# Optimization experiments

Hardware: AMD Instinct MI355X
Metric: run time of the kernel (lower is better)

Reference implementation:

```python
import jax, jax.numpy as jnp
import numpy as np

B, S, D, H, I = 4, 1024, 2048, 16, 8192
HD = D // H
S_IMG = 576
EPS = 1e-5


def _layer_norm(x, w, b):
    mu = jnp.mean(x, axis=-1, keepdims=True)
    var = jnp.var(x, axis=-1, keepdims=True)
    return (x - mu) * jax.lax.rsqrt(var + EPS) * w + b


def setup_inputs() -> dict:
    key = jax.random.key(0)
    ks = jax.random.split(key, 12)
    s = 0.02
    return {
        "image_features": jax.random.normal(ks[0], (B, S_IMG, D), jnp.float32),
        "hidden_states": jax.random.normal(ks[1], (B, S, D), jnp.float32),
        "attention_mask": jnp.ones((B, S), jnp.float32),
        "causal_attention_mask": jnp.zeros((B, 1, S, S), jnp.float32),
        "Wq": jax.random.normal(ks[2], (D, D), jnp.float32) * s,
        "bq": jnp.zeros((D,), jnp.float32),
        "Wk": jax.random.normal(ks[3], (D, D), jnp.float32) * s,
        "bk": jnp.zeros((D,), jnp.float32),
        "Wv": jax.random.normal(ks[4], (D, D), jnp.float32) * s,
        "bv": jnp.zeros((D,), jnp.float32),
        "Wo": jax.random.normal(ks[5], (D, D), jnp.float32) * s,
        "bo": jnp.zeros((D,), jnp.float32),
        "ln1_w": jnp.ones((D,), jnp.float32),
        "ln1_b": jnp.zeros((D,), jnp.float32),
        "ln2_w": jnp.ones((D,), jnp.float32),
        "ln2_b": jnp.zeros((D,), jnp.float32),
        "W1": jax.random.normal(ks[6], (I, D), jnp.float32) * s,
        "b1": jnp.zeros((I,), jnp.float32),
        "W2": jax.random.normal(ks[7], (D, I), jnp.float32) * s,
        "b2": jnp.zeros((D,), jnp.float32),
    }


def reference(image_features, hidden_states, attention_mask, causal_attention_mask,
              Wq, bq, Wk, bk, Wv, bv, Wo, bo,
              ln1_w, ln1_b, ln2_w, ln2_b, W1, b1, W2, b2):
    dtype = hidden_states.dtype
    scale = HD ** (-0.5)
    # expand_mask: [B,S] -> additive mask [B,1,S,S]
    inverted = 1.0 - attention_mask[:, None, None, :].astype(dtype)  # [B,1,1,S]
    add_mask = jnp.where(inverted.astype(bool), jnp.finfo(dtype).min, inverted)
    add_mask = jnp.broadcast_to(add_mask, (B, 1, S, S))

    residual = hidden_states
    x = _layer_norm(hidden_states, ln1_w, ln1_b)

    q = (x @ Wq.T + bq) * scale
    k = x @ Wk.T + bk
    v = x @ Wv.T + bv
    q = q.reshape(B, S, H, HD)
    k = k.reshape(B, S, H, HD)
    v = v.reshape(B, S, H, HD)

    scores = jnp.einsum('bqhd,bkhd->bhqk', q, k) + add_mask  # [B,H,S,S]
    probs = jax.nn.softmax(scores, axis=-1)
    attn = jnp.einsum('bhqk,bkhd->bqhd', probs, v).reshape(B, S, D)
    attn = attn @ Wo.T + bo

    hidden = residual + attn
    residual = hidden
    y = _layer_norm(hidden, ln2_w, ln2_b)
    y = jax.nn.gelu(y @ W1.T + b1, approximate=False)
    y = y @ W2.T + b2
    return residual + y
```

## Files before the change

kernel.cpp:

```cpp
#include <hip/hip_runtime.h>
#include <hip/hip_bf16.h>
#include <math.h>

typedef __hip_bfloat16 bf16;
typedef __attribute__((ext_vector_type(8))) short short8;
typedef __attribute__((ext_vector_type(4))) float floatx4;

constexpr int Bc = 4, Sc = 1024, Dc = 2048, Hc = 16, HDc = 128, Ic = 8192;
constexpr int QKVLD = 3 * Dc;

__device__ __forceinline__ float bf2f(bf16 x){ return __bfloat162float(x); }
__device__ __forceinline__ bf16 f2bf(float x){ return __float2bfloat16(x); }

__device__ __forceinline__ uint4 pack8(float4 a, float4 b){
    union { uint4 u; bf16 h[8]; } r;
    r.h[0]=f2bf(a.x); r.h[1]=f2bf(a.y); r.h[2]=f2bf(a.z); r.h[3]=f2bf(a.w);
    r.h[4]=f2bf(b.x); r.h[5]=f2bf(b.y); r.h[6]=f2bf(b.z); r.h[7]=f2bf(b.w);
    return r.u;
}

__device__ __forceinline__ void glds16(void* lds, const void* g){
    __builtin_amdgcn_global_load_lds(
        (__attribute__((address_space(1))) void*)(size_t)g,
        (__attribute__((address_space(3))) void*)lds,
        16, 0, 0);
}

__global__ __launch_bounds__(256)
void conv_w(const float* __restrict__ src, bf16* __restrict__ dst){
    const size_t i = ((size_t)blockIdx.x * 256 + threadIdx.x) * 8;
    float4 a = *(const float4*)(src + i);
    float4 b = *(const float4*)(src + i + 4);
    *(uint4*)(dst + i) = pack8(a, b);
}

template<int INF32>
__global__ __launch_bounds__(256)
void ln_kernel(const void* __restrict__ x, const float* __restrict__ w,
               const float* __restrict__ b, bf16* __restrict__ y)
{
    const int row = blockIdx.x;
    const int t = threadIdx.x;
    float f[8], s = 0.f, s2 = 0.f;
    if (INF32) {
        const float* xr = (const float*)x + (size_t)row * Dc + t * 8;
        float4 a = *(const float4*)xr, c = *(const float4*)(xr + 4);
        f[0]=a.x; f[1]=a.y; f[2]=a.z; f[3]=a.w; f[4]=c.x; f[5]=c.y; f[6]=c.z; f[7]=c.w;
    } else {
        union { uint4 u; bf16 h[8]; } ld;
        ld.u = *(const uint4*)((const bf16*)x + (size_t)row * Dc + t * 8);
#pragma unroll
        for (int j = 0; j < 8; ++j) f[j] = bf2f(ld.h[j]);
    }
#pragma unroll
    for (int j = 0; j < 8; ++j) { s += f[j]; s2 += f[j] * f[j]; }
#pragma unroll
    for (int off = 32; off; off >>= 1) { s += __shfl_xor(s, off); s2 += __shfl_xor(s2, off); }
    __shared__ float red[8];
    const int wave = t >> 6, lane = t & 63;
    if (lane == 0) { red[wave] = s; red[4 + wave] = s2; }
    __syncthreads();
    s  = red[0] + red[1] + red[2] + red[3];
    s2 = red[4] + red[5] + red[6] + red[7];
    const float mean = s * (1.0f / Dc);
    const float var  = s2 * (1.0f / Dc) - mean * mean;
    const float rs   = rsqrtf(var + 1e-5f);
    union { uint4 u; bf16 h[8]; } st;
#pragma unroll
    for (int j = 0; j < 8; ++j) {
        const int col = t * 8 + j;
        st.h[j] = f2bf((f[j] - mean) * rs * w[col] + b[col]);
    }
    *(uint4*)&y[(size_t)row * Dc + t * 8] = st.u;
}

template<int EPI, int RESF32, int OUTF32>
__global__ __launch_bounds__(256)
void gemm_bt(const bf16* __restrict__ A, const bf16* __restrict__ W,
             const float* __restrict__ bias, const float* __restrict__ bias2,
             const float* __restrict__ bias3, const void* __restrict__ res,
             void* __restrict__ C, int M, int N, int K, float scale)
{
    __shared__ __align__(16) bf16 As[128 * 32];
    __shared__ __align__(16) bf16 Bs[128 * 32];
    const int tile_m = blockIdx.y * 128;
    const int tile_n = blockIdx.x * 128;
    const int t = threadIdx.x;
    const int wave = t >> 6, lane = t & 63, quad = lane >> 4, l16 = lane & 15;
    const int wm = (wave >> 1) * 64, wn = (wave & 1) * 64;

    floatx4 acc[4][4] = {};

    const bf16* Ag  = A + (size_t)(tile_m + (t >> 2)) * K + (t & 3) * 8;
    const bf16* Ag2 = Ag + (size_t)64 * K;
    const bf16* Wg  = W + (size_t)(tile_n + (t >> 2)) * K + (t & 3) * 8;
    const bf16* Wg2 = Wg + (size_t)64 * K;
    char* AsB = (char*)As;
    char* BsB = (char*)Bs;
    const int wbase = wave * 1024;

    for (int k0 = 0; k0 < K; k0 += 32) {
        __syncthreads();
        glds16(AsB + wbase,        Ag  + k0);
        glds16(AsB + 4096 + wbase, Ag2 + k0);
        glds16(BsB + wbase,        Wg  + k0);
        glds16(BsB + 4096 + wbase, Wg2 + k0);
        __syncthreads();
        short8 af[4], bfr[4];
#pragma unroll
        for (int mi = 0; mi < 4; ++mi)
            af[mi] = *(const short8*)&As[(wm + mi * 16 + l16) * 32 + quad * 8];
#pragma unroll
        for (int ni = 0; ni < 4; ++ni)
            bfr[ni] = *(const short8*)&Bs[(wn + ni * 16 + l16) * 32 + quad * 8];
#pragma unroll
        for (int mi = 0; mi < 4; ++mi)
#pragma unroll
            for (int ni = 0; ni < 4; ++ni)
                acc[mi][ni] = __builtin_amdgcn_mfma_f32_16x16x32_bf16(af[mi], bfr[ni], acc[mi][ni], 0, 0, 0);
    }

#pragma unroll
    for (int mi = 0; mi < 4; ++mi) {
        const int row0 = tile_m + wm + mi * 16 + quad * 4;
#pragma unroll
        for (int ni = 0; ni < 4; ++ni) {
            const int col = tile_n + wn + ni * 16 + l16;
            float bv, sc = 1.f;
            if (EPI == 4) {
                if (col < 2048)      { bv = bias[col];         sc = scale; }
                else if (col < 4096) { bv = bias2[col - 2048]; }
                else                 { bv = bias3[col - 4096]; }
            } else {
                bv = bias[col];
            }
#pragma unroll
            for (int r = 0; r < 4; ++r) {
                float v = acc[mi][ni][r] + bv;
                if (EPI == 1) v *= scale;
                if (EPI == 4) v *= sc;
                if (EPI == 2) v = 0.5f * v * (1.0f + erff(v * 0.70710678118f));
                const size_t idx = (size_t)(row0 + r) * N + col;
                if (EPI == 3) v += RESF32 ? ((const float*)res)[idx] : bf2f(((const bf16*)res)[idx]);
                if (OUTF32) ((float*)C)[idx] = v;
                else        ((bf16*)C)[idx] = f2bf(v);
            }
        }
    }
}

__global__ __launch_bounds__(256)
void flash_attn(const bf16* __restrict__ QKV, const float* __restrict__ mask,
                bf16* __restrict__ O)
{
    __shared__ __align__(16) bf16 Ks[4 * 64 * 32];
    __shared__ __align__(16) bf16 Vt[128 * 72];
    __shared__ __align__(16) bf16 Ps[4][16 * 72];
    const int bh = blockIdx.y, b = bh >> 4, h = bh & 15;
    const int t = threadIdx.x, w = t >> 6, lane = t & 63, quad = lane >> 4, l16 = lane & 15;
    const int qbase = blockIdx.x * 64 + w * 16;
    const size_t rowb = (size_t)b * Sc;
    const bf16* Kp = QKV + 2048 + (size_t)h * HDc;
    const bf16* Vp = QKV + 4096 + (size_t)h * HDc;

    short8 qf[4];
    {
        const bf16* qp = QKV + (rowb + qbase + l16) * QKVLD + (size_t)h * HDc + quad * 8;
#pragma unroll
        for (int kc = 0; kc < 4; ++kc) qf[kc] = *(const short8*)(qp + kc * 32);
    }
    float m_i[4], l_i[4];
    floatx4 Oacc[8] = {};
#pragma unroll
    for (int r = 0; r < 4; ++r) { m_i[r] = -1e30f; l_i[r] = 0.f; }

    const int p2 = t & 31, dg = t >> 5;

    for (int kt = 0; kt < Sc; kt += 64) {
        __syncthreads();
#pragma unroll
        for (int u = 0; u < 4; ++u) {
            const int row = u * 16 + (lane >> 2);
            glds16((char*)Ks + w * 4096 + u * 1024,
                   Kp + (rowb + kt + row) * QKVLD + w * 32 + (lane & 3) * 8);
        }
        {
            union { uint4 u4; unsigned short s[8]; } va[2][2];
#pragma unroll
            for (int kk = 0; kk < 2; ++kk) {
                const bf16* vp = Vp + (rowb + kt + 2 * p2 + kk) * QKVLD + dg * 16;
                va[kk][0].u4 = *(const uint4*)vp;
                va[kk][1].u4 = *(const uint4*)(vp + 8);
            }
            unsigned* VtW = (unsigned*)Vt;
#pragma unroll
            for (int j = 0; j < 16; ++j) {
                const unsigned word = (unsigned)va[0][j >> 3].s[j & 7]
                                    | ((unsigned)va[1][j >> 3].s[j & 7] << 16);
                VtW[(dg * 16 + j) * 36 + p2] = word;
            }
        }
        __syncthreads();

        floatx4 sacc[4] = {};
#pragma unroll
        for (int kc = 0; kc < 4; ++kc)
#pragma unroll
            for (int sub = 0; sub < 4; ++sub) {
                short8 kf = *(const short8*)&Ks[kc * 2048 + (sub * 16 + l16) * 32 + quad * 8];
                sacc[sub] = __builtin_amdgcn_mfma_f32_16x16x32_bf16(qf[kc], kf, sacc[sub], 0, 0, 0);
            }
#pragma unroll
        for (int sub = 0; sub < 4; ++sub) {
            const float mv = mask[b * Sc + kt + sub * 16 + l16];
            const float madd = (mv < 0.5f) ? -3.0e38f : 0.f;
#pragma unroll
            for (int r = 0; r < 4; ++r) sacc[sub][r] += madd;
        }
        float p[4][4], alpha[4];
#pragma unroll
        for (int r = 0; r < 4; ++r) {
            float mx = fmaxf(fmaxf(sacc[0][r], sacc[1][r]), fmaxf(sacc[2][r], sacc[3][r]));
#pragma unroll
            for (int off = 8; off; off >>= 1) mx = fmaxf(mx, __shfl_xor(mx, off));
            const float mnew = fmaxf(m_i[r], mx);
            alpha[r] = exp2f(m_i[r] - mnew);
            float ps = 0.f;
#pragma unroll
            for (int sub = 0; sub < 4; ++sub) { p[sub][r] = exp2f(sacc[sub][r] - mnew); ps += p[sub][r]; }
#pragma unroll
            for (int off = 8; off; off >>= 1) ps += __shfl_xor(ps, off);
            l_i[r] = l_i[r] * alpha[r] + ps;
            m_i[r] = mnew;
        }
#pragma unroll
        for (int nsub = 0; nsub < 8; ++nsub)
#pragma unroll
            for (int r = 0; r < 4; ++r) Oacc[nsub][r] *= alpha[r];

        bf16* Pw = Ps[w];
#pragma unroll
        for (int sub = 0; sub < 4; ++sub)
#pragma unroll
            for (int r = 0; r < 4; ++r)
                Pw[(quad * 4 + r) * 72 + sub * 16 + l16] = f2bf(p[sub][r]);
        const short8 pf0 = *(const short8*)&Pw[l16 * 72 + quad * 8];
        const short8 pf1 = *(const short8*)&Pw[l16 * 72 + 32 + quad * 8];
#pragma unroll
        for (int nsub = 0; nsub < 8; ++nsub) {
            const short8 vf0 = *(const short8*)&Vt[(nsub * 16 + l16) * 72 + quad * 8];
            const short8 vf1 = *(const short8*)&Vt[(nsub * 16 + l16) * 72 + 32 + quad * 8];
            Oacc[nsub] = __builtin_amdgcn_mfma_f32_16x16x32_bf16(pf0, vf0, Oacc[nsub], 0, 0, 0);
            Oacc[nsub] = __builtin_amdgcn_mfma_f32_16x16x32_bf16(pf1, vf1, Oacc[nsub], 0, 0, 0);
        }
    }

#pragma unroll
    for (int r = 0; r < 4; ++r) {
        const float inv = 1.f / l_i[r];
        bf16* orow = O + (rowb + qbase + quad * 4 + r) * Dc + (size_t)h * HDc;
#pragma unroll
        for (int nsub = 0; nsub < 8; ++nsub)
            orow[nsub * 16 + l16] = f2bf(Oacc[nsub][r] * inv);
    }
}

extern "C" void kernel_launch(void* const* d_in, const int* in_sizes, int n_in,
                              void* d_out, int out_size, void* d_ws, size_t ws_size,
                              hipStream_t stream)
{
    const float* hidden = (const float*)d_in[1];
    const float* amask  = (const float*)d_in[2];
    const float* Wq = (const float*)d_in[4];  const float* bq = (const float*)d_in[5];
    const float* Wk = (const float*)d_in[6];  const float* bk = (const float*)d_in[7];
    const float* Wv = (const float*)d_in[8];  const float* bv = (const float*)d_in[9];
    const float* Wo = (const float*)d_in[10]; const float* bo = (const float*)d_in[11];
    const float* ln1w = (const float*)d_in[12]; const float* ln1b = (const float*)d_in[13];
    const float* ln2w = (const float*)d_in[14]; const float* ln2b = (const float*)d_in[15];
    const float* W1 = (const float*)d_in[16]; const float* b1 = (const float*)d_in[17];
    const float* W2 = (const float*)d_in[18]; const float* b2 = (const float*)d_in[19];

    const size_t UE = 8ull * 1024 * 1024;
    const size_t WE = 4ull * 1024 * 1024;
    bf16* U = (bf16*)d_ws;
    bf16* qkv   = U;
    bf16* wbuf  = U + 4 * UE;
    bf16* x_ln  = U + 6 * UE;
    bf16* hid2  = U + 6 * UE;
    bf16* ffn1  = U;
    bf16* attn  = (bf16*)d_out;
    bf16* y_ln  = (bf16*)d_out + UE;

    const float qscale = 0.08838834764831845f * 1.4426950408889634f;
    const dim3 gQKV(QKVLD / 128, Bc * Sc / 128);
    const dim3 gSq (Dc / 128,    Bc * Sc / 128);
    const dim3 gF1 (Ic / 128,    Bc * Sc / 128);

    conv_w<<<2048, 256, 0, stream>>>(Wq, wbuf);
    conv_w<<<2048, 256, 0, stream>>>(Wk, wbuf + WE);
    conv_w<<<2048, 256, 0, stream>>>(Wv, wbuf + 2 * WE);
    conv_w<<<2048, 256, 0, stream>>>(Wo, wbuf + 3 * WE);
    ln_kernel<1><<<Bc * Sc, 256, 0, stream>>>(hidden, ln1w, ln1b, x_ln);
    gemm_bt<4,0,0><<<gQKV, 256, 0, stream>>>(x_ln, wbuf, bq, bk, bv, nullptr, qkv,
                                             Bc * Sc, QKVLD, Dc, qscale);
    flash_attn<<<dim3(Sc / 64, Bc * Hc), 256, 0, stream>>>(qkv, amask, attn);
    gemm_bt<3,1,0><<<gSq, 256, 0, stream>>>(attn, wbuf + 3 * WE, bo, nullptr, nullptr, hidden, hid2,
                                            Bc * Sc, Dc, Dc, 0.f);
    ln_kernel<0><<<Bc * Sc, 256, 0, stream>>>(hid2, ln2w, ln2b, y_ln);
    conv_w<<<8192, 256, 0, stream>>>(W1, wbuf);
    gemm_bt<2,0,0><<<gF1, 256, 0, stream>>>(y_ln, wbuf, b1, nullptr, nullptr, nullptr, ffn1,
                                            Bc * Sc, Ic, Dc, 0.f);
    conv_w<<<8192, 256, 0, stream>>>(W2, wbuf);
    gemm_bt<3,0,1><<<gSq, 256, 0, stream>>>(ffn1, wbuf, b2, nullptr, nullptr, hid2, d_out,
                                            Bc * Sc, Dc, Ic, 0.f);
}
```

Baseline: 994.4 us.

## Split-K GEMMs with atomic accumulation, widen K tile with swizzled LDS

The two N=2048 GEMMs (output projection and FFN down) now use split-K over two z-slices. Each slice atomically adds fp32 partial sums into a buffer pre-filled with residual plus bias by a new init_add kernel. This gives those launches twice as many blocks on the device. The GEMM K-tile grows from 32 to 64, with an XOR-style swizzled LDS layout to cut bank conflicts and halve the barrier count per K step. The four attention weight conversions are also fused into one launch, and the intermediate hidden state is kept in fp32. In exchange, split-K adds atomic traffic, extra init passes and non-deterministic summation order.

```diff
diff --git a/kernel.cpp b/kernel.cpp
--- a/kernel.cpp
+++ b/kernel.cpp
@@ -32,6 +32,33 @@
     float4 a = *(const float4*)(src + i);
     float4 b = *(const float4*)(src + i + 4);
     *(uint4*)(dst + i) = pack8(a, b);
+}
+
+__global__ __launch_bounds__(256)
+void conv_w4(const float* __restrict__ s0, const float* __restrict__ s1,
+             const float* __restrict__ s2, const float* __restrict__ s3,
+             bf16* __restrict__ dst){
+    const int id = blockIdx.x >> 11;
+    const float* src = (id == 0) ? s0 : (id == 1) ? s1 : (id == 2) ? s2 : s3;
+    const size_t i = ((size_t)(blockIdx.x & 2047) * 256 + threadIdx.x) * 8;
+    float4 a = *(const float4*)(src + i);
+    float4 b = *(const float4*)(src + i + 4);
+    *(uint4*)(dst + (size_t)id * Dc * Dc + i) = pack8(a, b);
+}
+
+__global__ __launch_bounds__(256)
+void init_add(float* __restrict__ dst, const float* __restrict__ bias,
+              const float* __restrict__ src){
+    const size_t i = ((size_t)blockIdx.x * 256 + threadIdx.x) * 8;
+    const int col = (int)(i & (Dc - 1));
+    float4 a = *(const float4*)(src + i);
+    float4 b = *(const float4*)(src + i + 4);
+    float4 ba = *(const float4*)(bias + col);
+    float4 bb = *(const float4*)(bias + col + 4);
+    a.x += ba.x; a.y += ba.y; a.z += ba.z; a.w += ba.w;
+    b.x += bb.x; b.y += bb.y; b.z += bb.z; b.w += bb.w;
+    *(float4*)(dst + i) = a;
+    *(float4*)(dst + i + 4) = b;
 }
 
 template<int INF32>
@@ -81,43 +108,48 @@
              const float* __restrict__ bias3, const void* __restrict__ res,
              void* __restrict__ C, int M, int N, int K, float scale)
 {
-    __shared__ __align__(16) bf16 As[128 * 32];
-    __shared__ __align__(16) bf16 Bs[128 * 32];
+    __shared__ __align__(16) bf16 As[128 * 64];
+    __shared__ __align__(16) bf16 Bs[128 * 64];
     const int tile_m = blockIdx.y * 128;
     const int tile_n = blockIdx.x * 128;
     const int t = threadIdx.x;
     const int wave = t >> 6, lane = t & 63, quad = lane >> 4, l16 = lane & 15;
     const int wm = (wave >> 1) * 64, wn = (wave & 1) * 64;
+    const int Klen = K / gridDim.z, kbeg = blockIdx.z * Klen;
 
     floatx4 acc[4][4] = {};
 
-    const bf16* Ag  = A + (size_t)(tile_m + (t >> 2)) * K + (t & 3) * 8;
-    const bf16* Ag2 = Ag + (size_t)64 * K;
-    const bf16* Wg  = W + (size_t)(tile_n + (t >> 2)) * K + (t & 3) * 8;
-    const bf16* Wg2 = Wg + (size_t)64 * K;
+    const int r8 = t >> 3, c8 = t & 7;
+    const int cg = (c8 - r8) & 7;
+    const bf16* Ab = A + (size_t)(tile_m + r8) * K + kbeg + cg * 8;
+    const bf16* Wb = W + (size_t)(tile_n + r8) * K + kbeg + cg * 8;
     char* AsB = (char*)As;
     char* BsB = (char*)Bs;
-    const int wbase = wave * 1024;
-
-    for (int k0 = 0; k0 < K; k0 += 32) {
+    const int wb = wave * 1024;
+
+    for (int k0 = 0; k0 < Klen; k0 += 64) {
         __syncthreads();
-        glds16(AsB + wbase,        Ag  + k0);
-        glds16(AsB + 4096 + wbase, Ag2 + k0);
-        glds16(BsB + wbase,        Wg  + k0);
-        glds16(BsB + 4096 + wbase, Wg2 + k0);
+#pragma unroll
+        for (int u = 0; u < 4; ++u) {
+            glds16(AsB + u * 4096 + wb, Ab + (size_t)(u * 32) * K + k0);
+            glds16(BsB + u * 4096 + wb, Wb + (size_t)(u * 32) * K + k0);
+        }
         __syncthreads();
-        short8 af[4], bfr[4];
-#pragma unroll
-        for (int mi = 0; mi < 4; ++mi)
-            af[mi] = *(const short8*)&As[(wm + mi * 16 + l16) * 32 + quad * 8];
-#pragma unroll
-        for (int ni = 0; ni < 4; ++ni)
-            bfr[ni] = *(const short8*)&Bs[(wn + ni * 16 + l16) * 32 + quad * 8];
-#pragma unroll
-        for (int mi = 0; mi < 4; ++mi)
+#pragma unroll
+        for (int ks = 0; ks < 2; ++ks) {
+            short8 af[4], bfr[4];
+#pragma unroll
+            for (int mi = 0; mi < 4; ++mi)
+                af[mi] = *(const short8*)&As[(wm + mi * 16 + l16) * 64 + ((ks * 4 + quad + l16) & 7) * 8];
 #pragma unroll
             for (int ni = 0; ni < 4; ++ni)
-                acc[mi][ni] = __builtin_amdgcn_mfma_f32_16x16x32_bf16(af[mi], bfr[ni], acc[mi][ni], 0, 0, 0);
+                bfr[ni] = *(const short8*)&Bs[(wn + ni * 16 + l16) * 64 + ((ks * 4 + quad + l16) & 7) * 8];
+#pragma unroll
+            for (int mi = 0; mi < 4; ++mi)
+#pragma unroll
+                for (int ni = 0; ni < 4; ++ni)
+                    acc[mi][ni] = __builtin_amdgcn_mfma_f32_16x16x32_bf16(af[mi], bfr[ni], acc[mi][ni], 0, 0, 0);
+        }
     }
 
 #pragma unroll
@@ -126,21 +158,23 @@
 #pragma unroll
         for (int ni = 0; ni < 4; ++ni) {
             const int col = tile_n + wn + ni * 16 + l16;
-            float bv, sc = 1.f;
+            float bv = 0.f, sc = 1.f;
             if (EPI == 4) {
                 if (col < 2048)      { bv = bias[col];         sc = scale; }
                 else if (col < 4096) { bv = bias2[col - 2048]; }
                 else                 { bv = bias3[col - 4096]; }
-            } else {
+            } else if (EPI != 5) {
                 bv = bias[col];
             }
 #pragma unroll
             for (int r = 0; r < 4; ++r) {
-                float v = acc[mi][ni][r] + bv;
+                const size_t idx = (size_t)(row0 + r) * N + col;
+                float v = acc[mi][ni][r];
+                if (EPI == 5) { atomicAdd(&((float*)C)[idx], v); continue; }
+                v += bv;
                 if (EPI == 1) v *= scale;
                 if (EPI == 4) v *= sc;
                 if (EPI == 2) v = 0.5f * v * (1.0f + erff(v * 0.70710678118f));
-                const size_t idx = (size_t)(row0 + r) * N + col;
                 if (EPI == 3) v += RESF32 ? ((const float*)res)[idx] : bf2f(((const bf16*)res)[idx]);
                 if (OUTF32) ((float*)C)[idx] = v;
                 else        ((bf16*)C)[idx] = f2bf(v);
@@ -282,35 +316,35 @@
 
     const size_t UE = 8ull * 1024 * 1024;
     const size_t WE = 4ull * 1024 * 1024;
-    bf16* U = (bf16*)d_ws;
-    bf16* qkv   = U;
-    bf16* wbuf  = U + 4 * UE;
-    bf16* x_ln  = U + 6 * UE;
-    bf16* hid2  = U + 6 * UE;
-    bf16* ffn1  = U;
-    bf16* attn  = (bf16*)d_out;
-    bf16* y_ln  = (bf16*)d_out + UE;
+    bf16*  U = (bf16*)d_ws;
+    bf16*  qkv   = U;
+    bf16*  wbuf  = U + 4 * UE;
+    bf16*  x_ln  = U + 6 * UE;
+    float* hid2f = (float*)(U + 6 * UE);
+    bf16*  ffn1  = U;
+    bf16*  attn  = (bf16*)d_out;
+    bf16*  y_ln  = (bf16*)d_out + UE;
+    float* outf  = (float*)d_out;
 
     const float qscale = 0.08838834764831845f * 1.4426950408889634f;
-    const dim3 gQKV(QKVLD / 128, Bc * Sc / 128);
-    const dim3 gSq (Dc / 128,    Bc * Sc / 128);
-    const dim3 gF1 (Ic / 128,    Bc * Sc / 128);
-
-    conv_w<<<2048, 256, 0, stream>>>(Wq, wbuf);
-    conv_w<<<2048, 256, 0, stream>>>(Wk, wbuf + WE);
-    conv_w<<<2048, 256, 0, stream>>>(Wv, wbuf + 2 * WE);
-    conv_w<<<2048, 256, 0, stream>>>(Wo, wbuf + 3 * WE);
+    const dim3 gQKV(QKVLD / 128, Bc * Sc / 128, 1);
+    const dim3 gSK (Dc / 128,    Bc * Sc / 128, 2);
+    const dim3 gF1 (Ic / 128,    Bc * Sc / 128, 1);
+
+    conv_w4<<<8192, 256, 0, stream>>>(Wq, Wk, Wv, Wo, wbuf);
     ln_kernel<1><<<Bc * Sc, 256, 0, stream>>>(hidden, ln1w, ln1b, x_ln);
     gemm_bt<4,0,0><<<gQKV, 256, 0, stream>>>(x_ln, wbuf, bq, bk, bv, nullptr, qkv,
                                              Bc * Sc, QKVLD, Dc, qscale);
     flash_attn<<<dim3(Sc / 64, Bc * Hc), 256, 0, stream>>>(qkv, amask, attn);
-    gemm_bt<3,1,0><<<gSq, 256, 0, stream>>>(attn, wbuf + 3 * WE, bo, nullptr, nullptr, hidden, hid2,
-                                            Bc * Sc, Dc, Dc, 0.f);
-    ln_kernel<0><<<Bc * Sc, 256, 0, stream>>>(hid2, ln2w, ln2b, y_ln);
+    init_add<<<4096, 256, 0, stream>>>(hid2f, bo, hidden);
+    gemm_bt<5,0,1><<<gSK, 256, 0, stream>>>(attn, wbuf + 3 * WE, nullptr, nullptr, nullptr,
+                                            nullptr, hid2f, Bc * Sc, Dc, Dc, 0.f);
+    ln_kernel<1><<<Bc * Sc, 256, 0, stream>>>(hid2f, ln2w, ln2b, y_ln);
     conv_w<<<8192, 256, 0, stream>>>(W1, wbuf);
     gemm_bt<2,0,0><<<gF1, 256, 0, stream>>>(y_ln, wbuf, b1, nullptr, nullptr, nullptr, ffn1,
                                             Bc * Sc, Ic, Dc, 0.f);
+    init_add<<<4096, 256, 0, stream>>>(outf, b2, hid2f);
     conv_w<<<8192, 256, 0, stream>>>(W2, wbuf);
-    gemm_bt<3,0,1><<<gSq, 256, 0, stream>>>(ffn1, wbuf, b2, nullptr, nullptr, hid2, d_out,
-                                            Bc * Sc, Dc, Ic, 0.f);
-}
+    gemm_bt<5,0,1><<<gSK, 256, 0, stream>>>(ffn1, wbuf, nullptr, nullptr, nullptr,
+                                            nullptr, outf, Bc * Sc, Dc, Ic, 0.f);
+}
```

After: 990.8 us. About the same (-0.4%).
